# Optimization experiments

Hardware: AMD Instinct MI355X
Metric: run time of the kernel (lower is better)

The kernel has to match this reference:

```python
import jax, jax.numpy as jnp
import numpy as np
from jax import lax

N_WIRES = 4
EPS_BN = 1e-5

def _conv(x, w, b):
    y = lax.conv_general_dilated(x, w, (1, 1), 'SAME',
                                 dimension_numbers=('NCHW', 'OIHW', 'NCHW'))
    return y + b[None, :, None, None]

def _bn2d(x, g, b):
    mu = jnp.mean(x, axis=(0, 2, 3), keepdims=True)
    var = jnp.var(x, axis=(0, 2, 3), keepdims=True)
    return (x - mu) * lax.rsqrt(var + EPS_BN) * g[None, :, None, None] + b[None, :, None, None]

def _maxpool2(x):
    return lax.reduce_window(x, -jnp.inf, lax.max, (1, 1, 2, 2), (1, 1, 2, 2), 'VALID')

def _ry(t):
    c, s = jnp.cos(t / 2), jnp.sin(t / 2)
    return jnp.stack([jnp.stack([c, -s], -1), jnp.stack([s, c], -1)], -2).astype(jnp.complex64)

def _rz(t):
    tc = t.astype(jnp.complex64)
    em, ep = jnp.exp(-0.5j * tc), jnp.exp(0.5j * tc)
    z = jnp.zeros_like(em)
    return jnp.stack([jnpp_stack := jnp.stack([em, z], -1), jnp.stack([z, ep], -1)], -2)

def _rx(t):
    c = jnp.cos(t / 2).astype(jnp.complex64)
    s = (-1j) * jnp.sin(t / 2).astype(jnp.complex64)
    return jnp.stack([jnp.stack([c, s], -1), jnp.stack([s, c], -1)], -2)

def _apply_1q(state, U, q):
    # state: (B,2,2,2,2); U: (2,2) shared or (B,2,2) per-sample
    a = jnp.moveaxis(state, 1 + q, 1)
    if U.ndim == 2:
        a = jnp.einsum('ij,bj...->bi...', U, a)
    else:
        a = jnp.einsum('bij,bj...->bi...', U, a)
    return jnp.moveaxis(a, 1, 1 + q)

def _cnot(state, c, t):
    a = jnp.moveaxis(state, (1 + c, 1 + t), (1, 2))
    a = jnp.stack([a[:, 0], jnp.flip(a[:, 1], axis=1)], axis=1)
    return jnp.moveaxis(a, (1, 2), (1 + c, 1 + t))

def _circuit(scaled, theta, rho):
    # scaled: (B, 4) angles; theta, rho: (4, 3)
    B = scaled.shape[0]
    state = jnp.zeros((B,) + (2,) * N_WIRES, jnp.complex64)
    state = state.at[(slice(None),) + (0,) * N_WIRES].set(1.0 + 0j)
    for i in range(N_WIRES):
        state = _apply_1q(state, _ry(scaled[:, i]), i)
    for i in range(N_WIRES):
        state = _apply_1q(state, _ry(theta[i, 0]), i)
        state = _apply_1q(state, _rz(theta[i, 1]), i)
        state = _apply_1q(state, _rx(theta[i, 2]), i)
    for i in range(N_WIRES - 1):
        state = _cnot(state, i, i + 1)
    for i in range(N_WIRES):
        state = _apply_1q(state, _ry(rho[i, 0]), i)
        state = _apply_1q(state, _rz(rho[i, 1]), i)
        state = _apply_1q(state, _rx(rho[i, 2]), i)
    for i in range(N_WIRES - 1):
        state = _cnot(state, i + 1, i)
    probs = jnp.abs(state) ** 2  # (B,2,2,2,2)
    exps = []
    for i in range(N_WIRES):
        p = jnp.moveaxis(probs, 1 + i, 1)
        exps.append(jnp.sum(p[:, 0], axis=(1, 2, 3)) - jnp.sum(p[:, 1], axis=(1, 2, 3)))
    return jnp.stack(exps, axis=1)  # (B,4)

def setup_inputs() -> dict:
    key = jax.random.key(0)
    ks = jax.random.split(key, 8)
    B = 128
    return {
        'x': jax.random.normal(ks[0], (B, 1, 224, 224), jnp.float32),
        'conv1_w': jax.random.normal(ks[1], (8, 1, 3, 3), jnp.float32) * 0.1,
        'conv1_b': jnp.zeros((8,), jnp.float32),
        'bn1_g': jnp.ones((8,), jnp.float32),
        'bn1_b': jnp.zeros((8,), jnp.float32),
        'conv2_w': jax.random.normal(ks[2], (16, 8, 3, 3), jnp.float32) * 0.1,
        'conv2_b': jnp.zeros((16,), jnp.float32),
        'bn2_g': jnp.ones((16,), jnp.float32),
        'bn2_b': jnp.zeros((16,), jnp.float32),
        'theta': jax.random.normal(ks[3], (4, 3), jnp.float32),
        'rho': jax.random.normal(ks[4], (4, 3), jnp.float32),
        'norm_g': jnp.ones((4,), jnp.float32),
        'norm_b': jnp.zeros((4,), jnp.float32),
    }

def reference(x, conv1_w, conv1_b, bn1_g, bn1_b, conv2_w, conv2_b, bn2_g, bn2_b,
              theta, rho, norm_g, norm_b):
    h = jax.nn.relu(_bn2d(_conv(x, conv1_w, conv1_b), bn1_g, bn1_b))
    h = _maxpool2(h)
    h = jax.nn.relu(_bn2d(_conv(h, conv2_w, conv2_b), bn2_g, bn2_b))
    h = _maxpool2(h)
    feat = jnp.mean(h, axis=(2, 3))          # AdaptiveAvgPool2d((1,1)) + flatten -> (B,16)
    feat = feat[:, :N_WIRES]                  # (B,4)
    scaled = (feat - jnp.mean(feat)) / (jnp.std(feat, ddof=1) + 1e-6) * jnp.pi
    out = _circuit(scaled, theta, rho)        # (B,4) real
    mu = jnp.mean(out, axis=0, keepdims=True)
    var = jnp.var(out, axis=0, keepdims=True)
    return (out - mu) * lax.rsqrt(var + EPS_BN) * norm_g[None, :] + norm_b[None, :]
```

## Files before the change

kernel.cpp:

```cpp
#include <hip/hip_runtime.h>
#include <math.h>

#define H1 224
#define W1 224
#define H2 112
#define W2 112
#define HP 56
#define WP 56

#define NS 32
#define SLOT_STRIDE 64

struct C2 { float re, im; };
__device__ __forceinline__ C2 cmul(C2 a, C2 b) {
    return C2{fmaf(a.re, b.re, -a.im * b.im), fmaf(a.re, b.im, a.im * b.re)};
}
__device__ __forceinline__ C2 cadd(C2 a, C2 b) { return C2{a.re + b.re, a.im + b.im}; }

template <int S>
__device__ __forceinline__ void ap1s(C2* st, C2 u00, C2 u01, C2 u10, C2 u11) {
#pragma unroll
    for (int i = 0; i < 16; i++) {
        if (i & S) continue;
        C2 a0 = st[i], a1 = st[i + S];
        st[i]     = cadd(cmul(u00, a0), cmul(u01, a1));
        st[i + S] = cadd(cmul(u10, a0), cmul(u11, a1));
    }
}
template <int SC, int STT>
__device__ __forceinline__ void cnot_s(C2* st) {
#pragma unroll
    for (int i = 0; i < 16; i++)
        if ((i & SC) && !(i & STT)) { C2 t = st[i]; st[i] = st[i + STT]; st[i + STT] = t; }
}
struct M2 { C2 m[2][2]; };
__device__ __forceinline__ M2 mmul(const M2& A, const M2& B) {
    M2 R;
#pragma unroll
    for (int i = 0; i < 2; i++)
#pragma unroll
        for (int j = 0; j < 2; j++)
            R.m[i][j] = cadd(cmul(A.m[i][0], B.m[0][j]), cmul(A.m[i][1], B.m[1][j]));
    return R;
}
__device__ __forceinline__ M2 combined_u(const float* __restrict__ p) {
    float c0 = cosf(0.5f * p[0]), s0 = sinf(0.5f * p[0]);
    float c1 = cosf(0.5f * p[1]), s1 = sinf(0.5f * p[1]);
    float c2 = cosf(0.5f * p[2]), s2 = sinf(0.5f * p[2]);
    M2 Ry = {{{{c0, 0.f}, {-s0, 0.f}}, {{s0, 0.f}, {c0, 0.f}}}};
    M2 Rz = {{{{c1, -s1}, {0.f, 0.f}}, {{0.f, 0.f}, {c1, s1}}}};
    M2 Rx = {{{{c2, 0.f}, {0.f, -s2}}, {{0.f, -s2}, {c2, 0.f}}}};
    return mmul(Rx, mmul(Rz, Ry));
}

template <int Q>
__device__ __forceinline__ void rows_reduce(float* red, const float* vals, int tid) {
#pragma unroll
    for (int q = 0; q < Q; q++) red[q * 256 + tid] = vals[q];
    __syncthreads();
#pragma unroll
    for (int s = 128; s > 0; s >>= 1) {
        for (int idx = tid; idx < Q * s; idx += 256) {
            int row = idx / s, i = idx - row * s;
            red[row * 256 + i] += red[row * 256 + i + s];
        }
        __syncthreads();
    }
}

__global__ void zero_ws(float* ws, int n) {
    int i = blockIdx.x * blockDim.x + threadIdx.x;
    if (i < n) ws[i] = 0.f;
}

__device__ __forceinline__ float slot_sum(const float* stats, int c) {
    float s = 0.f;
#pragma unroll
    for (int sl = 0; sl < NS; sl++) s += stats[sl * SLOT_STRIDE + c];
    return s;
}

__global__ __launch_bounds__(256, 2) void conv1_pool_stats(
        const float* __restrict__ x, const float* __restrict__ w,
        const float* __restrict__ bias, const float* __restrict__ g1,
        float* __restrict__ stats1p, float* __restrict__ p1ext) {
    __shared__ float red[16 * 256];
    int strip = blockIdx.x;
    int b = blockIdx.y;
    int tid = threadIdx.x;
    int pc = tid & 127;
    int rhalf = tid >> 7;
    int r0 = strip * 16 + rhalf * 8;
    const float* xb = x + (size_t)b * H1 * W1;
    float sums[8], sqs[8], pm[8];
    bool gp[8];
#pragma unroll
    for (int c = 0; c < 8; c++) { sums[c] = 0.f; sqs[c] = 0.f; gp[c] = g1[c] >= 0.f; }
    bool act = pc < W2;
    if (act) {
        bool cl = pc > 0, cr = pc < W2 - 1;
        const float* rp0 = xb + (size_t)r0 * W1 + 2 * pc;
        float al, am0, am1, ar, bl, bm0, bm1, br;
        if (r0 > 0) {
            const float* rp = rp0 - W1;
            float2 m = *(const float2*)rp;
            al = cl ? rp[-1] : 0.f; am0 = m.x; am1 = m.y; ar = cr ? rp[2] : 0.f;
        } else { al = 0.f; am0 = 0.f; am1 = 0.f; ar = 0.f; }
        {
            float2 m = *(const float2*)rp0;
            bl = cl ? rp0[-1] : 0.f; bm0 = m.x; bm1 = m.y; br = cr ? rp0[2] : 0.f;
        }
#pragma unroll
        for (int rr = 0; rr < 8; rr++) {
            float nl = 0.f, nm0 = 0.f, nm1 = 0.f, nr = 0.f;
            int rn = r0 + rr + 1;
            if (rn < H1) {
                const float* rp = rp0 + (size_t)(rr + 1) * W1;
                float2 m = *(const float2*)rp;
                nl = cl ? rp[-1] : 0.f; nm0 = m.x; nm1 = m.y; nr = cr ? rp[2] : 0.f;
            }
            float4 e0 = make_float4(0.f, 0.f, 0.f, 0.f);
            float4 e1 = make_float4(0.f, 0.f, 0.f, 0.f);
#pragma unroll
            for (int c = 0; c < 8; c++) {
                const float* wc = w + c * 9;
                float y0 = bias[c], y1 = bias[c];
                y0 = fmaf(wc[0], al,  y0); y0 = fmaf(wc[1], am0, y0); y0 = fmaf(wc[2], am1, y0);
                y1 = fmaf(wc[0], am0, y1); y1 = fmaf(wc[1], am1, y1); y1 = fmaf(wc[2], ar,  y1);
                y0 = fmaf(wc[3], bl,  y0); y0 = fmaf(wc[4], bm0, y0); y0 = fmaf(wc[5], bm1, y0);
                y1 = fmaf(wc[3], bm0, y1); y1 = fmaf(wc[4], bm1, y1); y1 = fmaf(wc[5], br,  y1);
                y0 = fmaf(wc[6], nl,  y0); y0 = fmaf(wc[7], nm0, y0); y0 = fmaf(wc[8], nm1, y0);
                y1 = fmaf(wc[6], nm0, y1); y1 = fmaf(wc[7], nm1, y1); y1 = fmaf(wc[8], nr,  y1);
                sums[c] += y0 + y1;
                sqs[c] = fmaf(y0, y0, fmaf(y1, y1, sqs[c]));
                float m01 = gp[c] ? fmaxf(y0, y1) : fminf(y0, y1);
                if ((rr & 1) == 0) {
                    pm[c] = m01;
                } else {
                    float e = gp[c] ? fmaxf(pm[c], m01) : fminf(pm[c], m01);
                    if (c == 0) e0.x = e; else if (c == 1) e0.y = e;
                    else if (c == 2) e0.z = e; else if (c == 3) e0.w = e;
                    else if (c == 4) e1.x = e; else if (c == 5) e1.y = e;
                    else if (c == 6) e1.z = e; else e1.w = e;
                }
            }
            if (rr & 1) {
                int pr = (r0 + rr) >> 1;
                float* dst = p1ext + ((((size_t)b * H2 + pr) * W2 + pc) << 3);
                ((float4*)dst)[0] = e0;
                ((float4*)dst)[1] = e1;
            }
            al = bl; am0 = bm0; am1 = bm1; ar = br;
            bl = nl; bm0 = nm0; bm1 = nm1; br = nr;
        }
    }
    float vals[16];
#pragma unroll
    for (int c = 0; c < 8; c++) { vals[c] = sums[c]; vals[8 + c] = sqs[c]; }
    rows_reduce<16>(red, vals, tid);
    if (tid < 16) stats1p[((size_t)(b * 14 + strip) << 4) + tid] = red[tid * 256];
}

__global__ void conv1_stats(const float* __restrict__ x, const float* __restrict__ w,
                            const float* __restrict__ bias, float* __restrict__ stats) {
    __shared__ float red[16 * 256];
    int strip = blockIdx.x;
    int b = blockIdx.y;
    int tid = threadIdx.x;
    const float* xb = x + (size_t)b * H1 * W1;
    float sums[8], sqs[8];
#pragma unroll
    for (int c = 0; c < 8; c++) { sums[c] = 0.f; sqs[c] = 0.f; }
    int col = tid;
    if (col < W1) {
        bool cl = col > 0, cr = col < W1 - 1;
        int row0 = strip * 8;
        float a0, a1, a2, b0, b1, b2, c0, c1, c2;
        {
            int r = row0 - 1;
            if (r >= 0) {
                a0 = cl ? xb[r * W1 + col - 1] : 0.f;
                a1 = xb[r * W1 + col];
                a2 = cr ? xb[r * W1 + col + 1] : 0.f;
            } else { a0 = a1 = a2 = 0.f; }
            r = row0;
            b0 = cl ? xb[r * W1 + col - 1] : 0.f;
            b1 = xb[r * W1 + col];
            b2 = cr ? xb[r * W1 + col + 1] : 0.f;
        }
        for (int rr = 0; rr < 8; rr++) {
            int rn = row0 + rr + 1;
            if (rn < H1) {
                c0 = cl ? xb[rn * W1 + col - 1] : 0.f;
                c1 = xb[rn * W1 + col];
                c2 = cr ? xb[rn * W1 + col + 1] : 0.f;
            } else { c0 = c1 = c2 = 0.f; }
#pragma unroll
            for (int c = 0; c < 8; c++) {
                float acc = bias[c];
                acc = fmaf(w[c * 9 + 0], a0, acc);
                acc = fmaf(w[c * 9 + 1], a1, acc);
                acc = fmaf(w[c * 9 + 2], a2, acc);
                acc = fmaf(w[c * 9 + 3], b0, acc);
                acc = fmaf(w[c * 9 + 4], b1, acc);
                acc = fmaf(w[c * 9 + 5], b2, acc);
                acc = fmaf(w[c * 9 + 6], c0, acc);
                acc = fmaf(w[c * 9 + 7], c1, acc);
                acc = fmaf(w[c * 9 + 8], c2, acc);
                sums[c] += acc;
                sqs[c] = fmaf(acc, acc, sqs[c]);
            }
            a0 = b0; a1 = b1; a2 = b2;
            b0 = c0; b1 = c1; b2 = c2;
        }
    }
    float vals[16];
#pragma unroll
    for (int c = 0; c < 8; c++) { vals[c] = sums[c]; vals[8 + c] = sqs[c]; }
    rows_reduce<16>(red, vals, tid);
    int slot = (b * 28 + strip) & (NS - 1);
    if (tid < 16) atomicAdd(stats + slot * SLOT_STRIDE + tid, red[tid * 256]);
}

template <int PH, int PW>
__device__ __forceinline__ void build_h1_tile(const float* __restrict__ xb,
                                              float (*h1t)[PH][PW],
                                              const float* __restrict__ w1,
                                              const float* __restrict__ b1,
                                              const float* sc1, const float* sh1,
                                              int oy0, int ox0, int tid) {
    for (int i = tid; i < PH * PW; i += 256) {
        int p = i / PW, q = i % PW;
        int hy = oy0 + p, hx = ox0 + q;
        bool ok = (hy >= 0 && hy < H2 && hx >= 0 && hx < W2);
        float xp[5][5];
        if (hy >= 1 && hy <= H2 - 2 && hx >= 1 && hx <= W2 - 2) {
            const float* bp = xb + (2 * hy - 1) * W1 + (2 * hx - 1);
#pragma unroll
            for (int r = 0; r < 5; r++)
#pragma unroll
                for (int c = 0; c < 5; c++) xp[r][c] = bp[r * W1 + c];
        } else if (ok) {
#pragma unroll
            for (int r = 0; r < 5; r++)
#pragma unroll
                for (int c = 0; c < 5; c++) {
                    int gy = 2 * hy - 1 + r, gx = 2 * hx - 1 + c;
                    xp[r][c] = (gy >= 0 && gy < H1 && gx >= 0 && gx < W1) ? xb[gy * W1 + gx] : 0.f;
                }
        }
#pragma unroll
        for (int c = 0; c < 8; c++) {
            float mx = 0.f;
            if (ok) {
                mx = -INFINITY;
#pragma unroll
                for (int dy = 0; dy < 2; dy++)
#pragma unroll
                    for (int dx = 0; dx < 2; dx++) {
                        float acc = b1[c];
#pragma unroll
                        for (int ky = 0; ky < 3; ky++)
#pragma unroll
                            for (int kx = 0; kx < 3; kx++)
                                acc = fmaf(w1[c * 9 + ky * 3 + kx], xp[dy + ky][dx + kx], acc);
                        mx = fmaxf(mx, fmaxf(fmaf(acc, sc1[c], sh1[c]), 0.f));
                    }
            }
            h1t[c][p][q] = mx;
        }
    }
}

__global__ __launch_bounds__(256, 4) void conv2_stats_slim(
        const float* __restrict__ p1ext, const float* __restrict__ g1,
        const float* __restrict__ be1, const float* __restrict__ stats1p, int nblk1,
        const float* __restrict__ w2, const float* __restrict__ b2,
        const float* __restrict__ g2,
        float* __restrict__ stats2p, float* __restrict__ p2ext, float N1) {
    __shared__ __align__(16) float h1t[8][34][34];
    __shared__ float sc1[8], sh1[8];
    int b = blockIdx.z;
    int Y0 = blockIdx.y * 32, X0 = blockIdx.x * 32;
    int ty = threadIdx.y, tx = threadIdx.x;
    int tid = ty * 16 + tx;
    {
        float* scr = (float*)h1t;
        const float4* sp = (const float4*)stats1p;
        int tot4 = nblk1 << 2;
        float4 a0 = make_float4(0.f, 0.f, 0.f, 0.f);
        float4 a1 = a0, a2 = a0, a3 = a0;
        int idx = tid;
        for (; idx + 768 < tot4; idx += 1024) {
            float4 t0 = sp[idx];
            float4 t1 = sp[idx + 256];
            float4 t2 = sp[idx + 512];
            float4 t3 = sp[idx + 768];
            a0.x += t0.x; a0.y += t0.y; a0.z += t0.z; a0.w += t0.w;
            a1.x += t1.x; a1.y += t1.y; a1.z += t1.z; a1.w += t1.w;
            a2.x += t2.x; a2.y += t2.y; a2.z += t2.z; a2.w += t2.w;
            a3.x += t3.x; a3.y += t3.y; a3.z += t3.z; a3.w += t3.w;
        }
        for (; idx < tot4; idx += 256) {
            float4 t = sp[idx];
            a0.x += t.x; a0.y += t.y; a0.z += t.z; a0.w += t.w;
        }
        a0.x += a1.x + a2.x + a3.x;
        a0.y += a1.y + a2.y + a3.y;
        a0.z += a1.z + a2.z + a3.z;
        a0.w += a1.w + a2.w + a3.w;
        ((float4*)scr)[tid] = a0;
        __syncthreads();
        if (tid < 16) {
            int hi = tid >> 2, lo = tid & 3;
            float s = 0.f;
#pragma unroll
            for (int k = 0; k < 64; k++) s += scr[(((hi + (k << 2))) << 2) + lo];
            scr[1024 + tid] = s;
        }
        __syncthreads();
        if (tid < 8) {
            float su = scr[1024 + tid], sq = scr[1024 + 8 + tid];
            float mu = su / N1;
            float var = sq / N1 - mu * mu;
            float sc = g1[tid] * rsqrtf(var + 1e-5f);
            sc1[tid] = sc;
            sh1[tid] = be1[tid] - mu * sc;
        }
        __syncthreads();
    }
    const float* pb = p1ext + (((size_t)b * H2) * W2 << 3);
    for (int i = tid; i < 34 * 34; i += 256) {
        int p = i / 34, q = i % 34;
        int hy = Y0 - 1 + p, hx = X0 - 1 + q;
        if (hy >= 0 && hy < H2 && hx >= 0 && hx < W2) {
            const float* cp = pb + (((size_t)hy * W2 + hx) << 3);
            float4 u = ((const float4*)cp)[0];
            float4 v = ((const float4*)cp)[1];
            h1t[0][p][q] = fmaxf(fmaf(u.x, sc1[0], sh1[0]), 0.f);
            h1t[1][p][q] = fmaxf(fmaf(u.y, sc1[1], sh1[1]), 0.f);
            h1t[2][p][q] = fmaxf(fmaf(u.z, sc1[2], sh1[2]), 0.f);
            h1t[3][p][q] = fmaxf(fmaf(u.w, sc1[3], sh1[3]), 0.f);
            h1t[4][p][q] = fmaxf(fmaf(v.x, sc1[4], sh1[4]), 0.f);
            h1t[5][p][q] = fmaxf(fmaf(v.y, sc1[5], sh1[5]), 0.f);
            h1t[6][p][q] = fmaxf(fmaf(v.z, sc1[6], sh1[6]), 0.f);
            h1t[7][p][q] = fmaxf(fmaf(v.w, sc1[7], sh1[7]), 0.f);
        } else {
#pragma unroll
            for (int c = 0; c < 8; c++) h1t[c][p][q] = 0.f;
        }
    }
    __syncthreads();
    float acc[4][2][2];
#pragma unroll
    for (int co = 0; co < 4; co++)
#pragma unroll
        for (int dy = 0; dy < 2; dy++)
#pragma unroll
            for (int dx = 0; dx < 2; dx++) acc[co][dy][dx] = b2[co];
#pragma unroll
    for (int ci = 0; ci < 8; ci++) {
        float win[4][4];
#pragma unroll
        for (int r = 0; r < 4; r++) {
            const float2* rp = (const float2*)&h1t[ci][2 * ty + r][2 * tx];
            float2 u = rp[0], v = rp[1];
            win[r][0] = u.x; win[r][1] = u.y; win[r][2] = v.x; win[r][3] = v.y;
        }
#pragma unroll
        for (int co = 0; co < 4; co++)
#pragma unroll
            for (int ky = 0; ky < 3; ky++)
#pragma unroll
                for (int kx = 0; kx < 3; kx++) {
                    float wv = w2[co * 72 + ci * 9 + ky * 3 + kx];
#pragma unroll
                    for (int dy = 0; dy < 2; dy++)
#pragma unroll
                        for (int dx = 0; dx < 2; dx++)
                            acc[co][dy][dx] = fmaf(wv, win[dy + ky][dx + kx], acc[co][dy][dx]);
                }
    }
    int cy0 = Y0 + 2 * ty, cx0 = X0 + 2 * tx;
    bool vy0 = cy0 < H2, vy1 = cy0 + 1 < H2, vx0 = cx0 < W2, vx1 = cx0 + 1 < W2;
    float vals[8];
#pragma unroll
    for (int co = 0; co < 4; co++) {
        float s = 0.f, q = 0.f;
        if (vy0 && vx0) { float a = acc[co][0][0]; s += a; q = fmaf(a, a, q); }
        if (vy0 && vx1) { float a = acc[co][0][1]; s += a; q = fmaf(a, a, q); }
        if (vy1 && vx0) { float a = acc[co][1][0]; s += a; q = fmaf(a, a, q); }
        if (vy1 && vx1) { float a = acc[co][1][1]; s += a; q = fmaf(a, a, q); }
        vals[co] = s;
        vals[4 + co] = q;
    }
    {
        int hy = (Y0 >> 1) + ty, hx = (X0 >> 1) + tx;
        if (hy < HP && hx < WP) {
#pragma unroll
            for (int co = 0; co < 4; co++) {
                float mx = fmaxf(fmaxf(acc[co][0][0], acc[co][0][1]),
                                 fmaxf(acc[co][1][0], acc[co][1][1]));
                float mn = fminf(fminf(acc[co][0][0], acc[co][0][1]),
                                 fminf(acc[co][1][0], acc[co][1][1]));
                p2ext[(((size_t)b * 4 + co) * HP + hy) * WP + hx] = (g2[co] >= 0.f) ? mx : mn;
            }
        }
    }
    __syncthreads();
    float* red = (float*)h1t;
    rows_reduce<8>(red, vals, tid);
    int blkid = (blockIdx.z * gridDim.y + blockIdx.y) * gridDim.x + blockIdx.x;
    if (tid < 8) stats2p[((size_t)blkid << 3) + tid] = red[tid * 256];
}

template <bool STORE>
__global__ __launch_bounds__(256, 4) void conv2_stats_fused(
        const float* __restrict__ x, const float* __restrict__ w1,
        const float* __restrict__ b1, const float* __restrict__ g1,
        const float* __restrict__ be1, const float* __restrict__ stats1,
        const float* __restrict__ w2, const float* __restrict__ b2,
        float* __restrict__ stats2,
        float* __restrict__ pmax, float* __restrict__ pmin, float N1) {
    __shared__ __align__(16) float h1t[8][34][34];
    __shared__ float sc1[8], sh1[8];
    int b = blockIdx.z;
    int Y0 = blockIdx.y * 32, X0 = blockIdx.x * 32;
    int ty = threadIdx.y, tx = threadIdx.x;
    int tid = ty * 16 + tx;
    if (tid < 8) {
        float su = slot_sum(stats1, tid), sq = slot_sum(stats1, 8 + tid);
        float mu = su / N1;
        float var = sq / N1 - mu * mu;
        float sc = g1[tid] * rsqrtf(var + 1e-5f);
        sc1[tid] = sc;
        sh1[tid] = be1[tid] - mu * sc;
    }
    __syncthreads();
    const float* xb = x + (size_t)b * H1 * W1;
    build_h1_tile<34, 34>(xb, h1t, w1, b1, sc1, sh1, Y0 - 1, X0 - 1, tid);
    __syncthreads();
    float acc[4][2][2];
#pragma unroll
    for (int co = 0; co < 4; co++)
#pragma unroll
        for (int dy = 0; dy < 2; dy++)
#pragma unroll
            for (int dx = 0; dx < 2; dx++) acc[co][dy][dx] = b2[co];
#pragma unroll
    for (int ci = 0; ci < 8; ci++) {
        float win[4][4];
#pragma unroll
        for (int r = 0; r < 4; r++) {
            const float2* rp = (const float2*)&h1t[ci][2 * ty + r][2 * tx];
            float2 u = rp[0], v = rp[1];
            win[r][0] = u.x; win[r][1] = u.y; win[r][2] = v.x; win[r][3] = v.y;
        }
#pragma unroll
        for (int co = 0; co < 4; co++)
#pragma unroll
            for (int ky = 0; ky < 3; ky++)
#pragma unroll
                for (int kx = 0; kx < 3; kx++) {
                    float wv = w2[co * 72 + ci * 9 + ky * 3 + kx];
#pragma unroll
                    for (int dy = 0; dy < 2; dy++)
#pragma unroll
                        for (int dx = 0; dx < 2; dx++)
                            acc[co][dy][dx] = fmaf(wv, win[dy + ky][dx + kx], acc[co][dy][dx]);
                }
    }
    int cy0 = Y0 + 2 * ty, cx0 = X0 + 2 * tx;
    bool vy0 = cy0 < H2, vy1 = cy0 + 1 < H2, vx0 = cx0 < W2, vx1 = cx0 + 1 < W2;
    float vals[8];
#pragma unroll
    for (int co = 0; co < 4; co++) {
        float s = 0.f, q = 0.f;
        if (vy0 && vx0) { float a = acc[co][0][0]; s += a; q = fmaf(a, a, q); }
        if (vy0 && vx1) { float a = acc[co][0][1]; s += a; q = fmaf(a, a, q); }
        if (vy1 && vx0) { float a = acc[co][1][0]; s += a; q = fmaf(a, a, q); }
        if (vy1 && vx1) { float a = acc[co][1][1]; s += a; q = fmaf(a, a, q); }
        vals[co] = s;
        vals[4 + co] = q;
    }
    if (STORE) {
        int hy = (Y0 >> 1) + ty, hx = (X0 >> 1) + tx;
        if (hy < HP && hx < WP) {
#pragma unroll
            for (int co = 0; co < 4; co++) {
                float mx = fmaxf(fmaxf(acc[co][0][0], acc[co][0][1]),
                                 fmaxf(acc[co][1][0], acc[co][1][1]));
                float mn = fminf(fminf(acc[co][0][0], acc[co][0][1]),
                                 fminf(acc[co][1][0], acc[co][1][1]));
                size_t idx = (((size_t)b * 4 + co) * HP + hy) * WP + hx;
                pmax[idx] = mx;
                pmin[idx] = mn;
            }
        }
    }
    __syncthreads();
    float* red = (float*)h1t;
    rows_reduce<8>(red, vals, tid);
    int slot = ((b * 16) + blockIdx.y * 4 + blockIdx.x) & (NS - 1);
    if (tid < 8) atomicAdd(stats2 + slot * SLOT_STRIDE + tid, red[tid * 256]);
}

__global__ void pool_bn_mean_p(const float* __restrict__ p2ext,
                               const float* __restrict__ g2, const float* __restrict__ be2,
                               const float* __restrict__ stats2p, int nblk2,
                               float* __restrict__ featbuf, float N2) {
    __shared__ float red[1024 + 16];
    int co = blockIdx.x & 3;
    int b = blockIdx.x >> 2;
    int tid = threadIdx.x;
    {
        const float4* sp = (const float4*)stats2p;
        int tot4 = nblk2 << 1;
        float4 a0 = make_float4(0.f, 0.f, 0.f, 0.f);
        float4 a1 = a0;
        int idx = tid;
        for (; idx + 256 < tot4; idx += 512) {
            float4 t0 = sp[idx];
            float4 t1 = sp[idx + 256];
            a0.x += t0.x; a0.y += t0.y; a0.z += t0.z; a0.w += t0.w;
            a1.x += t1.x; a1.y += t1.y; a1.z += t1.z; a1.w += t1.w;
        }
        for (; idx < tot4; idx += 256) {
            float4 t = sp[idx];
            a0.x += t.x; a0.y += t.y; a0.z += t.z; a0.w += t.w;
        }
        a0.x += a1.x; a0.y += a1.y; a0.z += a1.z; a0.w += a1.w;
        ((float4*)red)[tid] = a0;
    }
    __syncthreads();
    if (tid < 8) {
        int hi = tid >> 2, lo = tid & 3;
        float s = 0.f;
#pragma unroll
        for (int k = 0; k < 128; k++) s += red[((hi + (k << 1)) << 2) + lo];
        red[1024 + tid] = s;
    }
    __syncthreads();
    float su = red[1024 + co], sq = red[1024 + 4 + co];
    float mu = su / N2;
    float var = sq / N2 - mu * mu;
    float sc = g2[co] * rsqrtf(var + 1e-5f);
    float sh = be2[co] - mu * sc;
    const float4* P4 = (const float4*)(p2ext + ((size_t)b * 4 + co) * (HP * WP));
    float s = 0.f;
    for (int i = tid; i < (HP * WP) / 4; i += 256) {
        float4 t = P4[i];
        s += fmaxf(fmaf(t.x, sc, sh), 0.f) + fmaxf(fmaf(t.y, sc, sh), 0.f) +
             fmaxf(fmaf(t.z, sc, sh), 0.f) + fmaxf(fmaf(t.w, sc, sh), 0.f);
    }
    __syncthreads();
    red[tid] = s;
    __syncthreads();
    for (int st = 128; st > 0; st >>= 1) {
        if (tid < st) red[tid] += red[tid + st];
        __syncthreads();
    }
    if (tid == 0) featbuf[(size_t)b * 4 + co] = red[0];
}

__global__ void pool_bn_mean(const float* __restrict__ pmax, const float* __restrict__ pmin,
                             const float* __restrict__ g2, const float* __restrict__ be2,
                             const float* __restrict__ stats2,
                             float* __restrict__ featbuf, float N2) {
    __shared__ float red[256];
    int co = blockIdx.x & 3;
    int b = blockIdx.x >> 2;
    int tid = threadIdx.x;
    float su = slot_sum(stats2, co), sq = slot_sum(stats2, 4 + co);
    float mu = su / N2;
    float var = sq / N2 - mu * mu;
    float sc = g2[co] * rsqrtf(var + 1e-5f);
    float sh = be2[co] - mu * sc;
    const float* P = (sc >= 0.f ? pmax : pmin) + ((size_t)b * 4 + co) * (HP * WP);
    float s = 0.f;
    for (int i = tid; i < HP * WP; i += 256) s += fmaxf(fmaf(P[i], sc, sh), 0.f);
    red[tid] = s;
    __syncthreads();
    for (int st = 128; st > 0; st >>= 1) {
        if (tid < st) red[tid] += red[tid + st];
        __syncthreads();
    }
    if (tid == 0) featbuf[(size_t)b * 4 + co] = red[0];
}

__global__ void conv2_final_fused(const float* __restrict__ x, const float* __restrict__ w1,
                                  const float* __restrict__ b1, const float* __restrict__ g1,
                                  const float* __restrict__ be1,
                                  const float* __restrict__ stats1,
                                  const float* __restrict__ w2, const float* __restrict__ b2,
                                  const float* __restrict__ g2, const float* __restrict__ be2,
                                  const float* __restrict__ stats2,
                                  float* __restrict__ featbuf, float N1, float N2) {
    __shared__ __align__(16) float h1t[8][34][34];
    __shared__ float sc1[8], sh1[8];
    __shared__ float sc2[4], sh2[4];
    int b = blockIdx.z;
    int py0 = blockIdx.y * 16, px0 = blockIdx.x * 16;
    int ty = threadIdx.y, tx = threadIdx.x;
    int tid = ty * 16 + tx;
    if (tid < 8) {
        float su = slot_sum(stats1, tid), sq = slot_sum(stats1, 8 + tid);
        float mu = su / N1;
        float var = sq / N1 - mu * mu;
        float sc = g1[tid] * rsqrtf(var + 1e-5f);
        sc1[tid] = sc;
        sh1[tid] = be1[tid] - mu * sc;
    }
    if (tid >= 16 && tid < 20) {
        int j = tid - 16;
        float su = slot_sum(stats2, j), sq = slot_sum(stats2, 4 + j);
        float mu = su / N2;
        float var = sq / N2 - mu * mu;
        float sc = g2[j] * rsqrtf(var + 1e-5f);
        sc2[j] = sc;
        sh2[j] = be2[j] - mu * sc;
    }
    __syncthreads();
    const float* xb = x + (size_t)b * H1 * W1;
    build_h1_tile<34, 34>(xb, h1t, w1, b1, sc1, sh1, 2 * py0 - 1, 2 * px0 - 1, tid);
    __syncthreads();
    bool valid = (py0 + ty < HP) && (px0 + tx < WP);
    float acc[4][2][2];
#pragma unroll
    for (int co = 0; co < 4; co++)
#pragma unroll
        for (int dy = 0; dy < 2; dy++)
#pragma unroll
            for (int dx = 0; dx < 2; dx++) acc[co][dy][dx] = b2[co];
#pragma unroll
    for (int ci = 0; ci < 8; ci++) {
        float win[4][4];
#pragma unroll
        for (int r = 0; r < 4; r++) {
            const float2* rp = (const float2*)&h1t[ci][2 * ty + r][2 * tx];
            float2 u = rp[0], v = rp[1];
            win[r][0] = u.x; win[r][1] = u.y; win[r][2] = v.x; win[r][3] = v.y;
        }
#pragma unroll
        for (int co = 0; co < 4; co++)
#pragma unroll
            for (int ky = 0; ky < 3; ky++)
#pragma unroll
                for (int kx = 0; kx < 3; kx++) {
                    float wv = w2[co * 72 + ci * 9 + ky * 3 + kx];
#pragma unroll
                    for (int dy = 0; dy < 2; dy++)
#pragma unroll
                        for (int dx = 0; dx < 2; dx++)
                            acc[co][dy][dx] = fmaf(wv, win[dy + ky][dx + kx], acc[co][dy][dx]);
                }
    }
    float vals[4];
#pragma unroll
    for (int co = 0; co < 4; co++) {
        float mx = -INFINITY;
#pragma unroll
        for (int dy = 0; dy < 2; dy++)
#pragma unroll
            for (int dx = 0; dx < 2; dx++)
                mx = fmaxf(mx, fmaxf(fmaf(acc[co][dy][dx], sc2[co], sh2[co]), 0.f));
        vals[co] = valid ? mx : 0.f;
    }
    __syncthreads();
    float* red = (float*)h1t;
    rows_reduce<4>(red, vals, tid);
    if (tid < 4) atomicAdd(featbuf + (size_t)b * 4 + tid, red[tid * 256]);
}

__device__ __forceinline__ float bsum(float v, float* lds) {
#pragma unroll
    for (int off = 32; off; off >>= 1) v += __shfl_xor(v, off, 64);
    __syncthreads();
    if ((threadIdx.x & 63) == 0) lds[threadIdx.x >> 6] = v;
    __syncthreads();
    float r = 0.f;
    int nw = (int)(blockDim.x + 63) >> 6;
#pragma clang loop unroll(disable)
    for (int i = 0; i < nw; i++) r += lds[i];
    return r;
}

__global__ void finalize(const float* __restrict__ featbuf, const float* __restrict__ theta,
                         const float* __restrict__ rho, const float* __restrict__ ng,
                         const float* __restrict__ nb, float* __restrict__ out, int B) {
    __shared__ float lds[16];
    int b = threadIdx.x;
    float f[4];
#pragma unroll
    for (int j = 0; j < 4; j++) f[j] = featbuf[b * 4 + j] * (1.f / (HP * WP));
    float n = 4.f * (float)B;
    float mean = bsum(f[0] + f[1] + f[2] + f[3], lds) / n;
    float d2 = 0.f;
#pragma unroll
    for (int j = 0; j < 4; j++) { float d = f[j] - mean; d2 += d * d; }
    float var1 = bsum(d2, lds) / (n - 1.f);
    float stdv = sqrtf(fmaxf(var1, 0.f)) + 1e-6f;
    const float PI = 3.14159265358979323846f;
    float cs[4], sn[4];
#pragma unroll
    for (int j = 0; j < 4; j++) {
        float sc = (f[j] - mean) / stdv * PI;
        cs[j] = cosf(0.5f * sc);
        sn[j] = sinf(0.5f * sc);
    }
    C2 st[16];
    {
        float amp[16];
        amp[1] = sn[3]; amp[0] = cs[3];
#pragma unroll
        for (int k = 0; k < 2; k++) { amp[k + 2] = amp[k] * sn[2]; amp[k] *= cs[2]; }
#pragma unroll
        for (int k = 0; k < 4; k++) { amp[k + 4] = amp[k] * sn[1]; amp[k] *= cs[1]; }
#pragma unroll
        for (int k = 0; k < 8; k++) { amp[k + 8] = amp[k] * sn[0]; amp[k] *= cs[0]; }
#pragma unroll
        for (int i = 0; i < 16; i++) st[i] = C2{amp[i], 0.f};
    }
#pragma clang loop unroll(disable)
    for (int l = 0; l < 2; l++) {
        const float* p = (l == 0) ? theta : rho;
#pragma clang loop unroll(disable)
        for (int i = 0; i < 4; i++) {
            M2 U = combined_u(p + i * 3);
            switch (i) {
            case 0: ap1s<8>(st, U.m[0][0], U.m[0][1], U.m[1][0], U.m[1][1]); break;
            case 1: ap1s<4>(st, U.m[0][0], U.m[0][1], U.m[1][0], U.m[1][1]); break;
            case 2: ap1s<2>(st, U.m[0][0], U.m[0][1], U.m[1][0], U.m[1][1]); break;
            default: ap1s<1>(st, U.m[0][0], U.m[0][1], U.m[1][0], U.m[1][1]); break;
            }
        }
        if (l == 0) { cnot_s<8, 4>(st); cnot_s<4, 2>(st); cnot_s<2, 1>(st); }
        else        { cnot_s<4, 8>(st); cnot_s<2, 4>(st); cnot_s<1, 2>(st); }
    }
    float e[4];
#pragma unroll
    for (int qb = 0; qb < 4; qb++) {
        int m = 8 >> qb;
        float p0 = 0.f, p1 = 0.f;
#pragma unroll
        for (int i = 0; i < 16; i++) {
            float pr = st[i].re * st[i].re + st[i].im * st[i].im;
            if (i & m) p1 += pr; else p0 += pr;
        }
        e[qb] = p0 - p1;
    }
#pragma clang loop unroll(disable)
    for (int j = 0; j < 4; j++) {
        float mu = bsum(e[j], lds) / (float)B;
        float dv = e[j] - mu;
        float v = bsum(dv * dv, lds) / (float)B;
        out[b * 4 + j] = fmaf(dv, rsqrtf(v + 1e-5f) * ng[j], nb[j]);
    }
}

extern "C" void kernel_launch(void* const* d_in, const int* in_sizes, int n_in,
                              void* d_out, int out_size, void* d_ws, size_t ws_size,
                              hipStream_t stream) {
    const float* x     = (const float*)d_in[0];
    const float* w1    = (const float*)d_in[1];
    const float* b1    = (const float*)d_in[2];
    const float* g1    = (const float*)d_in[3];
    const float* be1   = (const float*)d_in[4];
    const float* w2    = (const float*)d_in[5];
    const float* b2    = (const float*)d_in[6];
    const float* g2    = (const float*)d_in[7];
    const float* be2   = (const float*)d_in[8];
    const float* theta = (const float*)d_in[9];
    const float* rho   = (const float*)d_in[10];
    const float* ng    = (const float*)d_in[11];
    const float* nb    = (const float*)d_in[12];
    float* out = (float*)d_out;

    int B = in_sizes[0] / (H1 * W1);

    float N1 = (float)B * H1 * W1;
    float N2 = (float)B * H2 * W2;

    int nblk1 = 14 * B;
    int nblk2 = 16 * B;

    size_t p2n = (size_t)B * 4 * HP * WP;
    size_t p1n = (size_t)B * 8 * H2 * W2;

    size_t offs1p = 0;
    size_t offs2p = offs1p + (size_t)nblk1 * 16;
    size_t offfb  = offs2p + (size_t)nblk2 * 8;
    size_t offp2  = offfb + (size_t)B * 4;
    size_t offp1  = offp2 + p2n;
    size_t needA  = (offp1 + p1n) * sizeof(float);

    size_t common = (size_t)(2 * NS * SLOT_STRIDE) + (size_t)B * 4;
    size_t needB = (common + 2 * p2n) * sizeof(float);

    bool tierA = ws_size >= needA;
    bool tierB = !tierA && ws_size >= needB;

    float* ws = (float*)d_ws;

    if (tierA) {
        float* stats1p = ws + offs1p;
        float* stats2p = ws + offs2p;
        float* featbuf = ws + offfb;
        float* p2ext   = ws + offp2;
        float* p1ext   = ws + offp1;
        conv1_pool_stats<<<dim3(14, B), 256, 0, stream>>>(x, w1, b1, g1, stats1p, p1ext);
        conv2_stats_slim<<<dim3(4, 4, B), dim3(16, 16), 0, stream>>>(
            p1ext, g1, be1, stats1p, nblk1, w2, b2, g2, stats2p, p2ext, N1);
        pool_bn_mean_p<<<B * 4, 256, 0, stream>>>(p2ext, g2, be2, stats2p, nblk2, featbuf, N2);
        finalize<<<1, B, 0, stream>>>(featbuf, theta, rho, ng, nb, out, B);
    } else if (tierB) {
        float* stats1 = ws;
        float* stats2 = ws + NS * SLOT_STRIDE;
        float* featbuf = ws + 2 * NS * SLOT_STRIDE;
        float* bufs = featbuf + (size_t)B * 4;
        float* pmax = bufs;
        float* pmin = bufs + p2n;
        int nz = (int)common;
        zero_ws<<<(nz + 255) / 256, 256, 0, stream>>>(ws, nz);
        conv1_stats<<<dim3(28, B), 256, 0, stream>>>(x, w1, b1, stats1);
        conv2_stats_fused<true><<<dim3(4, 4, B), dim3(16, 16), 0, stream>>>(
            x, w1, b1, g1, be1, stats1, w2, b2, stats2, pmax, pmin, N1);
        pool_bn_mean<<<B * 4, 256, 0, stream>>>(pmax, pmin, g2, be2, stats2, featbuf, N2);
        finalize<<<1, B, 0, stream>>>(featbuf, theta, rho, ng, nb, out, B);
    } else {
        float* stats1 = ws;
        float* stats2 = ws + NS * SLOT_STRIDE;
        float* featbuf = ws + 2 * NS * SLOT_STRIDE;
        int nz = (int)common;
        zero_ws<<<(nz + 255) / 256, 256, 0, stream>>>(ws, nz);
        conv1_stats<<<dim3(28, B), 256, 0, stream>>>(x, w1, b1, stats1);
        conv2_stats_fused<false><<<dim3(4, 4, B), dim3(16, 16), 0, stream>>>(
            x, w1, b1, g1, be1, stats1, w2, b2, stats2, nullptr, nullptr, N1);
        conv2_final_fused<<<dim3(4, 4, B), dim3(16, 16), 0, stream>>>(
            x, w1, b1, g1, be1, stats1, w2, b2, g2, be2, stats2, featbuf, N1, N2);
        finalize<<<1, B, 0, stream>>>(featbuf, theta, rho, ng, nb, out, B);
    }
}
```

Before: 173.0 us.

## Fuse pipeline into single cooperative persistent kernel with grid syncs

Replaces the four-kernel tier-A pipeline (conv1+pool+stats, conv2+stats, pool/BN mean, finalize) with one cooperative kernel. It loops over work items per phase and separates phases with grid.sync, so per-launch overhead and inter-kernel gaps go away. BN1 affine terms are computed once by block 0 and broadcast through workspace instead of being recomputed in every conv2 block. The costs are grid-sync latency, idle blocks during the serial phases, and lower occupancy from the larger shared-memory footprint. Fallback launches of finalize now use 256 threads.

```diff
diff --git a/kernel.cpp b/kernel.cpp
--- a/kernel.cpp
+++ b/kernel.cpp
@@ -1,5 +1,8 @@
 #include <hip/hip_runtime.h>
+#include <hip/hip_cooperative_groups.h>
 #include <math.h>
+
+namespace cg = cooperative_groups;
 
 #define H1 224
 #define W1 224
@@ -80,22 +83,19 @@
     return s;
 }
 
-__global__ __launch_bounds__(256, 2) void conv1_pool_stats(
-        const float* __restrict__ x, const float* __restrict__ w,
-        const float* __restrict__ bias, const float* __restrict__ g1,
-        float* __restrict__ stats1p, float* __restrict__ p1ext) {
-    __shared__ float red[16 * 256];
-    int strip = blockIdx.x;
-    int b = blockIdx.y;
-    int tid = threadIdx.x;
+
+__device__ __forceinline__ void conv1_item_body(
+        int b, int strip, const float* __restrict__ x, const float* __restrict__ w,
+        const float* __restrict__ bias, const bool* gp,
+        float* __restrict__ stats1p, float* __restrict__ p1ext,
+        float* red, int tid, int witem) {
     int pc = tid & 127;
     int rhalf = tid >> 7;
     int r0 = strip * 16 + rhalf * 8;
     const float* xb = x + (size_t)b * H1 * W1;
     float sums[8], sqs[8], pm[8];
-    bool gp[8];
-#pragma unroll
-    for (int c = 0; c < 8; c++) { sums[c] = 0.f; sqs[c] = 0.f; gp[c] = g1[c] >= 0.f; }
+#pragma unroll
+    for (int c = 0; c < 8; c++) { sums[c] = 0.f; sqs[c] = 0.f; }
     bool act = pc < W2;
     if (act) {
         bool cl = pc > 0, cr = pc < W2 - 1;
@@ -158,8 +158,449 @@
 #pragma unroll
     for (int c = 0; c < 8; c++) { vals[c] = sums[c]; vals[8 + c] = sqs[c]; }
     rows_reduce<16>(red, vals, tid);
-    if (tid < 16) stats1p[((size_t)(b * 14 + strip) << 4) + tid] = red[tid * 256];
-}
+    if (tid < 16) stats1p[((size_t)witem << 4) + tid] = red[tid * 256];
+}
+
+__device__ __forceinline__ void conv2_item_body(
+        int b, int Y0, int X0, const float* __restrict__ p1ext,
+        const float* sc1, const float* sh1,
+        const float* __restrict__ w2, const float* __restrict__ b2,
+        const float* __restrict__ g2,
+        float* __restrict__ stats2p, float* __restrict__ p2ext,
+        float* smem, int tid, int witem) {
+    float (*h1t)[34][34] = (float(*)[34][34])smem;
+    int ty = tid >> 4, tx = tid & 15;
+    const float* pb = p1ext + (((size_t)b * H2) * W2 << 3);
+    for (int i = tid; i < 34 * 34; i += 256) {
+        int p = i / 34, q = i % 34;
+        int hy = Y0 - 1 + p, hx = X0 - 1 + q;
+        if (hy >= 0 && hy < H2 && hx >= 0 && hx < W2) {
+            const float* cp = pb + (((size_t)hy * W2 + hx) << 3);
+            float4 u = ((const float4*)cp)[0];
+            float4 v = ((const float4*)cp)[1];
+            h1t[0][p][q] = fmaxf(fmaf(u.x, sc1[0], sh1[0]), 0.f);
+            h1t[1][p][q] = fmaxf(fmaf(u.y, sc1[1], sh1[1]), 0.f);
+            h1t[2][p][q] = fmaxf(fmaf(u.z, sc1[2], sh1[2]), 0.f);
+            h1t[3][p][q] = fmaxf(fmaf(u.w, sc1[3], sh1[3]), 0.f);
+            h1t[4][p][q] = fmaxf(fmaf(v.x, sc1[4], sh1[4]), 0.f);
+            h1t[5][p][q] = fmaxf(fmaf(v.y, sc1[5], sh1[5]), 0.f);
+            h1t[6][p][q] = fmaxf(fmaf(v.z, sc1[6], sh1[6]), 0.f);
+            h1t[7][p][q] = fmaxf(fmaf(v.w, sc1[7], sh1[7]), 0.f);
+        } else {
+#pragma unroll
+            for (int c = 0; c < 8; c++) h1t[c][p][q] = 0.f;
+        }
+    }
+    __syncthreads();
+    float acc[4][2][2];
+#pragma unroll
+    for (int co = 0; co < 4; co++)
+#pragma unroll
+        for (int dy = 0; dy < 2; dy++)
+#pragma unroll
+            for (int dx = 0; dx < 2; dx++) acc[co][dy][dx] = b2[co];
+#pragma unroll
+    for (int ci = 0; ci < 8; ci++) {
+        float win[4][4];
+#pragma unroll
+        for (int r = 0; r < 4; r++) {
+            const float2* rp = (const float2*)&h1t[ci][2 * ty + r][2 * tx];
+            float2 u = rp[0], v = rp[1];
+            win[r][0] = u.x; win[r][1] = u.y; win[r][2] = v.x; win[r][3] = v.y;
+        }
+#pragma unroll
+        for (int co = 0; co < 4; co++)
+#pragma unroll
+            for (int ky = 0; ky < 3; ky++)
+#pragma unroll
+                for (int kx = 0; kx < 3; kx++) {
+                    float wv = w2[co * 72 + ci * 9 + ky * 3 + kx];
+#pragma unroll
+                    for (int dy = 0; dy < 2; dy++)
+#pragma unroll
+                        for (int dx = 0; dx < 2; dx++)
+                            acc[co][dy][dx] = fmaf(wv, win[dy + ky][dx + kx], acc[co][dy][dx]);
+                }
+    }
+    int cy0 = Y0 + 2 * ty, cx0 = X0 + 2 * tx;
+    bool vy0 = cy0 < H2, vy1 = cy0 + 1 < H2, vx0 = cx0 < W2, vx1 = cx0 + 1 < W2;
+    float vals[8];
+#pragma unroll
+    for (int co = 0; co < 4; co++) {
+        float s = 0.f, q = 0.f;
+        if (vy0 && vx0) { float a = acc[co][0][0]; s += a; q = fmaf(a, a, q); }
+        if (vy0 && vx1) { float a = acc[co][0][1]; s += a; q = fmaf(a, a, q); }
+        if (vy1 && vx0) { float a = acc[co][1][0]; s += a; q = fmaf(a, a, q); }
+        if (vy1 && vx1) { float a = acc[co][1][1]; s += a; q = fmaf(a, a, q); }
+        vals[co] = s;
+        vals[4 + co] = q;
+    }
+    {
+        int hy = (Y0 >> 1) + ty, hx = (X0 >> 1) + tx;
+        if (hy < HP && hx < WP) {
+#pragma unroll
+            for (int co = 0; co < 4; co++) {
+                float mx = fmaxf(fmaxf(acc[co][0][0], acc[co][0][1]),
+                                 fmaxf(acc[co][1][0], acc[co][1][1]));
+                float mn = fminf(fminf(acc[co][0][0], acc[co][0][1]),
+                                 fminf(acc[co][1][0], acc[co][1][1]));
+                p2ext[(((size_t)b * 4 + co) * HP + hy) * WP + hx] = (g2[co] >= 0.f) ? mx : mn;
+            }
+        }
+    }
+    __syncthreads();
+    rows_reduce<8>(smem, vals, tid);
+    if (tid < 8) stats2p[((size_t)witem << 3) + tid] = smem[tid * 256];
+}
+
+__device__ __forceinline__ void pool_item_body(
+        int b, int co, const float* __restrict__ p2ext,
+        const float* __restrict__ g2, const float* __restrict__ be2,
+        const float* __restrict__ stats2p, int nblk2,
+        float* __restrict__ featbuf, float N2, float* red, int tid) {
+    {
+        const float4* sp = (const float4*)stats2p;
+        int tot4 = nblk2 << 1;
+        float4 a0 = make_float4(0.f, 0.f, 0.f, 0.f);
+        float4 a1 = a0;
+        int idx = tid;
+        for (; idx + 256 < tot4; idx += 512) {
+            float4 t0 = sp[idx];
+            float4 t1 = sp[idx + 256];
+            a0.x += t0.x; a0.y += t0.y; a0.z += t0.z; a0.w += t0.w;
+            a1.x += t1.x; a1.y += t1.y; a1.z += t1.z; a1.w += t1.w;
+        }
+        for (; idx < tot4; idx += 256) {
+            float4 t = sp[idx];
+            a0.x += t.x; a0.y += t.y; a0.z += t.z; a0.w += t.w;
+        }
+        a0.x += a1.x; a0.y += a1.y; a0.z += a1.z; a0.w += a1.w;
+        ((float4*)red)[tid] = a0;
+    }
+    __syncthreads();
+    if (tid < 8) {
+        int hi = tid >> 2, lo = tid & 3;
+        float s = 0.f;
+#pragma unroll
+        for (int k = 0; k < 128; k++) s += red[((hi + (k << 1)) << 2) + lo];
+        red[1024 + tid] = s;
+    }
+    __syncthreads();
+    float su = red[1024 + co], sq = red[1024 + 4 + co];
+    float mu = su / N2;
+    float var = sq / N2 - mu * mu;
+    float sc = g2[co] * rsqrtf(var + 1e-5f);
+    float sh = be2[co] - mu * sc;
+    const float4* P4 = (const float4*)(p2ext + ((size_t)b * 4 + co) * (HP * WP));
+    float s = 0.f;
+    for (int i = tid; i < (HP * WP) / 4; i += 256) {
+        float4 t = P4[i];
+        s += fmaxf(fmaf(t.x, sc, sh), 0.f) + fmaxf(fmaf(t.y, sc, sh), 0.f) +
+             fmaxf(fmaf(t.z, sc, sh), 0.f) + fmaxf(fmaf(t.w, sc, sh), 0.f);
+    }
+    __syncthreads();
+    red[tid] = s;
+    __syncthreads();
+    for (int st = 128; st > 0; st >>= 1) {
+        if (tid < st) red[tid] += red[tid + st];
+        __syncthreads();
+    }
+    if (tid == 0) featbuf[(size_t)b * 4 + co] = red[0];
+}
+
+__device__ __forceinline__ float bsum(float v, float* lds) {
+#pragma unroll
+    for (int off = 32; off; off >>= 1) v += __shfl_xor(v, off, 64);
+    __syncthreads();
+    if ((threadIdx.x & 63) == 0) lds[threadIdx.x >> 6] = v;
+    __syncthreads();
+    float r = 0.f;
+    int nw = (int)(blockDim.x + 63) >> 6;
+#pragma clang loop unroll(disable)
+    for (int i = 0; i < nw; i++) r += lds[i];
+    return r;
+}
+
+__device__ __forceinline__ void finalize_body(
+        const float* __restrict__ featbuf, const float* __restrict__ theta,
+        const float* __restrict__ rho, const float* __restrict__ ng,
+        const float* __restrict__ nb, float* __restrict__ out, int B, float* lds) {
+    int b = threadIdx.x;
+    bool act = b < B;
+    float f[4];
+#pragma unroll
+    for (int j = 0; j < 4; j++) f[j] = act ? featbuf[b * 4 + j] * (1.f / (HP * WP)) : 0.f;
+    float n = 4.f * (float)B;
+    float mean = bsum(f[0] + f[1] + f[2] + f[3], lds) / n;
+    float d2 = 0.f;
+    if (act) {
+#pragma unroll
+        for (int j = 0; j < 4; j++) { float d = f[j] - mean; d2 += d * d; }
+    }
+    float var1 = bsum(d2, lds) / (n - 1.f);
+    float stdv = sqrtf(fmaxf(var1, 0.f)) + 1e-6f;
+    const float PI = 3.14159265358979323846f;
+    float cs[4], sn[4];
+#pragma unroll
+    for (int j = 0; j < 4; j++) {
+        float sc = (f[j] - mean) / stdv * PI;
+        cs[j] = cosf(0.5f * sc);
+        sn[j] = sinf(0.5f * sc);
+    }
+    C2 st[16];
+    {
+        float amp[16];
+        amp[1] = sn[3]; amp[0] = cs[3];
+#pragma unroll
+        for (int k = 0; k < 2; k++) { amp[k + 2] = amp[k] * sn[2]; amp[k] *= cs[2]; }
+#pragma unroll
+        for (int k = 0; k < 4; k++) { amp[k + 4] = amp[k] * sn[1]; amp[k] *= cs[1]; }
+#pragma unroll
+        for (int k = 0; k < 8; k++) { amp[k + 8] = amp[k] * sn[0]; amp[k] *= cs[0]; }
+#pragma unroll
+        for (int i = 0; i < 16; i++) st[i] = C2{amp[i], 0.f};
+    }
+#pragma clang loop unroll(disable)
+    for (int l = 0; l < 2; l++) {
+        const float* p = (l == 0) ? theta : rho;
+#pragma clang loop unroll(disable)
+        for (int i = 0; i < 4; i++) {
+            M2 U = combined_u(p + i * 3);
+            switch (i) {
+            case 0: ap1s<8>(st, U.m[0][0], U.m[0][1], U.m[1][0], U.m[1][1]); break;
+            case 1: ap1s<4>(st, U.m[0][0], U.m[0][1], U.m[1][0], U.m[1][1]); break;
+            case 2: ap1s<2>(st, U.m[0][0], U.m[0][1], U.m[1][0], U.m[1][1]); break;
+            default: ap1s<1>(st, U.m[0][0], U.m[0][1], U.m[1][0], U.m[1][1]); break;
+            }
+        }
+        if (l == 0) { cnot_s<8, 4>(st); cnot_s<4, 2>(st); cnot_s<2, 1>(st); }
+        else        { cnot_s<4, 8>(st); cnot_s<2, 4>(st); cnot_s<1, 2>(st); }
+    }
+    float e[4];
+#pragma unroll
+    for (int qb = 0; qb < 4; qb++) {
+        int m = 8 >> qb;
+        float p0 = 0.f, p1 = 0.f;
+#pragma unroll
+        for (int i = 0; i < 16; i++) {
+            float pr = st[i].re * st[i].re + st[i].im * st[i].im;
+            if (i & m) p1 += pr; else p0 += pr;
+        }
+        e[qb] = p0 - p1;
+    }
+#pragma clang loop unroll(disable)
+    for (int j = 0; j < 4; j++) {
+        float mu = bsum(act ? e[j] : 0.f, lds) / (float)B;
+        float dv = e[j] - mu;
+        float v = bsum(act ? dv * dv : 0.f, lds) / (float)B;
+        if (act) out[b * 4 + j] = fmaf(dv, rsqrtf(v + 1e-5f) * ng[j], nb[j]);
+    }
+}
+
+__global__ __launch_bounds__(256, 4) void mega_all(
+        const float* __restrict__ x, const float* __restrict__ w1,
+        const float* __restrict__ b1, const float* __restrict__ g1,
+        const float* __restrict__ be1,
+        const float* __restrict__ w2, const float* __restrict__ b2,
+        const float* __restrict__ g2, const float* __restrict__ be2,
+        const float* __restrict__ theta, const float* __restrict__ rho,
+        const float* __restrict__ ng, const float* __restrict__ nb,
+        float* __restrict__ stats1p, float* __restrict__ stats2p,
+        float* __restrict__ aff1, float* __restrict__ featbuf,
+        float* __restrict__ p2ext, float* __restrict__ p1ext,
+        float* __restrict__ out, int B) {
+    cg::grid_group grid = cg::this_grid();
+    __shared__ __align__(16) float smem[8 * 34 * 34];
+    __shared__ float sc1s[8], sh1s[8];
+    int tid = threadIdx.x;
+    int bid = blockIdx.x;
+    int gsz = gridDim.x;
+    float N1 = (float)B * H1 * W1;
+    float N2 = (float)B * H2 * W2;
+
+    {
+        bool gp[8];
+#pragma unroll
+        for (int c = 0; c < 8; c++) gp[c] = g1[c] >= 0.f;
+        int n1 = 14 * B;
+        for (int w = bid; w < n1; w += gsz) {
+            __syncthreads();
+            int b = w / 14, strip = w - b * 14;
+            conv1_item_body(b, strip, x, w1, b1, gp, stats1p, p1ext, smem, tid, w);
+        }
+    }
+    __threadfence();
+    grid.sync();
+
+    if (bid == 0) {
+        float* scr = smem;
+        const float4* sp = (const float4*)stats1p;
+        int tot4 = (14 * B) << 2;
+        float4 a0 = make_float4(0.f, 0.f, 0.f, 0.f);
+        float4 a1 = a0, a2 = a0, a3 = a0;
+        int idx = tid;
+        for (; idx + 768 < tot4; idx += 1024) {
+            float4 t0 = sp[idx];
+            float4 t1 = sp[idx + 256];
+            float4 t2 = sp[idx + 512];
+            float4 t3 = sp[idx + 768];
+            a0.x += t0.x; a0.y += t0.y; a0.z += t0.z; a0.w += t0.w;
+            a1.x += t1.x; a1.y += t1.y; a1.z += t1.z; a1.w += t1.w;
+            a2.x += t2.x; a2.y += t2.y; a2.z += t2.z; a2.w += t2.w;
+            a3.x += t3.x; a3.y += t3.y; a3.z += t3.z; a3.w += t3.w;
+        }
+        for (; idx < tot4; idx += 256) {
+            float4 t = sp[idx];
+            a0.x += t.x; a0.y += t.y; a0.z += t.z; a0.w += t.w;
+        }
+        a0.x += a1.x + a2.x + a3.x;
+        a0.y += a1.y + a2.y + a3.y;
+        a0.z += a1.z + a2.z + a3.z;
+        a0.w += a1.w + a2.w + a3.w;
+        ((float4*)scr)[tid] = a0;
+        __syncthreads();
+        if (tid < 16) {
+            int hi = tid >> 2, lo = tid & 3;
+            float s = 0.f;
+#pragma unroll
+            for (int k = 0; k < 64; k++) s += scr[((hi + (k << 2)) << 2) + lo];
+            scr[1024 + tid] = s;
+        }
+        __syncthreads();
+        if (tid < 8) {
+            float su = scr[1024 + tid], sq = scr[1024 + 8 + tid];
+            float mu = su / N1;
+            float var = sq / N1 - mu * mu;
+            float sc = g1[tid] * rsqrtf(var + 1e-5f);
+            aff1[tid] = sc;
+            aff1[8 + tid] = be1[tid] - mu * sc;
+        }
+    }
+    __threadfence();
+    grid.sync();
+
+    {
+        if (tid < 8) { sc1s[tid] = aff1[tid]; sh1s[tid] = aff1[8 + tid]; }
+        __syncthreads();
+        int n2 = 16 * B;
+        for (int w = bid; w < n2; w += gsz) {
+            __syncthreads();
+            int b = w >> 4, t = w & 15;
+            conv2_item_body(b, (t >> 2) * 32, (t & 3) * 32, p1ext, sc1s, sh1s,
+                            w2, b2, g2, stats2p, p2ext, smem, tid, w);
+        }
+    }
+    __threadfence();
+    grid.sync();
+
+    {
+        int n3 = 4 * B;
+        for (int w = bid; w < n3; w += gsz) {
+            __syncthreads();
+            pool_item_body(w >> 2, w & 3, p2ext, g2, be2, stats2p, 16 * B,
+                           featbuf, N2, smem, tid);
+        }
+    }
+    __threadfence();
+    grid.sync();
+
+    if (bid == 0) {
+        __syncthreads();
+        finalize_body(featbuf, theta, rho, ng, nb, out, B, smem);
+    }
+}
+
+
+__global__ __launch_bounds__(256, 2) void conv1_pool_stats(
+        const float* __restrict__ x, const float* __restrict__ w,
+        const float* __restrict__ bias, const float* __restrict__ g1,
+        float* __restrict__ stats1p, float* __restrict__ p1ext) {
+    __shared__ float red[16 * 256];
+    int strip = blockIdx.x;
+    int b = blockIdx.y;
+    int tid = threadIdx.x;
+    bool gp[8];
+#pragma unroll
+    for (int c = 0; c < 8; c++) gp[c] = g1[c] >= 0.f;
+    conv1_item_body(b, strip, x, w, bias, gp, stats1p, p1ext, red, tid, b * 14 + strip);
+}
+
+__global__ __launch_bounds__(256, 4) void conv2_stats_slim(
+        const float* __restrict__ p1ext, const float* __restrict__ g1,
+        const float* __restrict__ be1, const float* __restrict__ stats1p, int nblk1,
+        const float* __restrict__ w2, const float* __restrict__ b2,
+        const float* __restrict__ g2,
+        float* __restrict__ stats2p, float* __restrict__ p2ext, float N1) {
+    __shared__ __align__(16) float smem[8 * 34 * 34];
+    __shared__ float sc1[8], sh1[8];
+    int b = blockIdx.z;
+    int tid = threadIdx.y * 16 + threadIdx.x;
+    {
+        float* scr = smem;
+        const float4* sp = (const float4*)stats1p;
+        int tot4 = nblk1 << 2;
+        float4 a0 = make_float4(0.f, 0.f, 0.f, 0.f);
+        float4 a1 = a0, a2 = a0, a3 = a0;
+        int idx = tid;
+        for (; idx + 768 < tot4; idx += 1024) {
+            float4 t0 = sp[idx];
+            float4 t1 = sp[idx + 256];
+            float4 t2 = sp[idx + 512];
+            float4 t3 = sp[idx + 768];
+            a0.x += t0.x; a0.y += t0.y; a0.z += t0.z; a0.w += t0.w;
+            a1.x += t1.x; a1.y += t1.y; a1.z += t1.z; a1.w += t1.w;
+            a2.x += t2.x; a2.y += t2.y; a2.z += t2.z; a2.w += t2.w;
+            a3.x += t3.x; a3.y += t3.y; a3.z += t3.z; a3.w += t3.w;
+        }
+        for (; idx < tot4; idx += 256) {
+            float4 t = sp[idx];
+            a0.x += t.x; a0.y += t.y; a0.z += t.z; a0.w += t.w;
+        }
+        a0.x += a1.x + a2.x + a3.x;
+        a0.y += a1.y + a2.y + a3.y;
+        a0.z += a1.z + a2.z + a3.z;
+        a0.w += a1.w + a2.w + a3.w;
+        ((float4*)scr)[tid] = a0;
+        __syncthreads();
+        if (tid < 16) {
+            int hi = tid >> 2, lo = tid & 3;
+            float s = 0.f;
+#pragma unroll
+            for (int k = 0; k < 64; k++) s += scr[((hi + (k << 2)) << 2) + lo];
+            scr[1024 + tid] = s;
+        }
+        __syncthreads();
+        if (tid < 8) {
+            float su = scr[1024 + tid], sq = scr[1024 + 8 + tid];
+            float mu = su / N1;
+            float var = sq / N1 - mu * mu;
+            float sc = g1[tid] * rsqrtf(var + 1e-5f);
+            sc1[tid] = sc;
+            sh1[tid] = be1[tid] - mu * sc;
+        }
+        __syncthreads();
+    }
+    int blkid = (blockIdx.z * gridDim.y + blockIdx.y) * gridDim.x + blockIdx.x;
+    conv2_item_body(b, blockIdx.y * 32, blockIdx.x * 32, p1ext, sc1, sh1,
+                    w2, b2, g2, stats2p, p2ext, smem, tid, blkid);
+}
+
+__global__ void pool_bn_mean_p(const float* __restrict__ p2ext,
+                               const float* __restrict__ g2, const float* __restrict__ be2,
+                               const float* __restrict__ stats2p, int nblk2,
+                               float* __restrict__ featbuf, float N2) {
+    __shared__ float red[1024 + 16];
+    pool_item_body(blockIdx.x >> 2, blockIdx.x & 3, p2ext, g2, be2, stats2p, nblk2,
+                   featbuf, N2, red, threadIdx.x);
+}
+
+__global__ void finalize(const float* __restrict__ featbuf, const float* __restrict__ theta,
+                         const float* __restrict__ rho, const float* __restrict__ ng,
+                         const float* __restrict__ nb, float* __restrict__ out, int B) {
+    __shared__ float lds[16];
+    finalize_body(featbuf, theta, rho, ng, nb, out, B, lds);
+}
+
 
 __global__ void conv1_stats(const float* __restrict__ x, const float* __restrict__ w,
                             const float* __restrict__ bias, float* __restrict__ stats) {
@@ -270,148 +711,6 @@
             h1t[c][p][q] = mx;
         }
     }
-}
-
-__global__ __launch_bounds__(256, 4) void conv2_stats_slim(
-        const float* __restrict__ p1ext, const float* __restrict__ g1,
-        const float* __restrict__ be1, const float* __restrict__ stats1p, int nblk1,
-        const float* __restrict__ w2, const float* __restrict__ b2,
-        const float* __restrict__ g2,
-        float* __restrict__ stats2p, float* __restrict__ p2ext, float N1) {
-    __shared__ __align__(16) float h1t[8][34][34];
-    __shared__ float sc1[8], sh1[8];
-    int b = blockIdx.z;
-    int Y0 = blockIdx.y * 32, X0 = blockIdx.x * 32;
-    int ty = threadIdx.y, tx = threadIdx.x;
-    int tid = ty * 16 + tx;
-    {
-        float* scr = (float*)h1t;
-        const float4* sp = (const float4*)stats1p;
-        int tot4 = nblk1 << 2;
-        float4 a0 = make_float4(0.f, 0.f, 0.f, 0.f);
-        float4 a1 = a0, a2 = a0, a3 = a0;
-        int idx = tid;
-        for (; idx + 768 < tot4; idx += 1024) {
-            float4 t0 = sp[idx];
-            float4 t1 = sp[idx + 256];
-            float4 t2 = sp[idx + 512];
-            float4 t3 = sp[idx + 768];
-            a0.x += t0.x; a0.y += t0.y; a0.z += t0.z; a0.w += t0.w;
-            a1.x += t1.x; a1.y += t1.y; a1.z += t1.z; a1.w += t1.w;
-            a2.x += t2.x; a2.y += t2.y; a2.z += t2.z; a2.w += t2.w;
-            a3.x += t3.x; a3.y += t3.y; a3.z += t3.z; a3.w += t3.w;
-        }
-        for (; idx < tot4; idx += 256) {
-            float4 t = sp[idx];
-            a0.x += t.x; a0.y += t.y; a0.z += t.z; a0.w += t.w;
-        }
-        a0.x += a1.x + a2.x + a3.x;
-        a0.y += a1.y + a2.y + a3.y;
-        a0.z += a1.z + a2.z + a3.z;
-        a0.w += a1.w + a2.w + a3.w;
-        ((float4*)scr)[tid] = a0;
-        __syncthreads();
-        if (tid < 16) {
-            int hi = tid >> 2, lo = tid & 3;
-            float s = 0.f;
-#pragma unroll
-            for (int k = 0; k < 64; k++) s += scr[(((hi + (k << 2))) << 2) + lo];
-            scr[1024 + tid] = s;
-        }
-        __syncthreads();
-        if (tid < 8) {
-            float su = scr[1024 + tid], sq = scr[1024 + 8 + tid];
-            float mu = su / N1;
-            float var = sq / N1 - mu * mu;
-            float sc = g1[tid] * rsqrtf(var + 1e-5f);
-            sc1[tid] = sc;
-            sh1[tid] = be1[tid] - mu * sc;
-        }
-        __syncthreads();
-    }
-    const float* pb = p1ext + (((size_t)b * H2) * W2 << 3);
-    for (int i = tid; i < 34 * 34; i += 256) {
-        int p = i / 34, q = i % 34;
-        int hy = Y0 - 1 + p, hx = X0 - 1 + q;
-        if (hy >= 0 && hy < H2 && hx >= 0 && hx < W2) {
-            const float* cp = pb + (((size_t)hy * W2 + hx) << 3);
-            float4 u = ((const float4*)cp)[0];
-            float4 v = ((const float4*)cp)[1];
-            h1t[0][p][q] = fmaxf(fmaf(u.x, sc1[0], sh1[0]), 0.f);
-            h1t[1][p][q] = fmaxf(fmaf(u.y, sc1[1], sh1[1]), 0.f);
-            h1t[2][p][q] = fmaxf(fmaf(u.z, sc1[2], sh1[2]), 0.f);
-            h1t[3][p][q] = fmaxf(fmaf(u.w, sc1[3], sh1[3]), 0.f);
-            h1t[4][p][q] = fmaxf(fmaf(v.x, sc1[4], sh1[4]), 0.f);
-            h1t[5][p][q] = fmaxf(fmaf(v.y, sc1[5], sh1[5]), 0.f);
-            h1t[6][p][q] = fmaxf(fmaf(v.z, sc1[6], sh1[6]), 0.f);
-            h1t[7][p][q] = fmaxf(fmaf(v.w, sc1[7], sh1[7]), 0.f);
-        } else {
-#pragma unroll
-            for (int c = 0; c < 8; c++) h1t[c][p][q] = 0.f;
-        }
-    }
-    __syncthreads();
-    float acc[4][2][2];
-#pragma unroll
-    for (int co = 0; co < 4; co++)
-#pragma unroll
-        for (int dy = 0; dy < 2; dy++)
-#pragma unroll
-            for (int dx = 0; dx < 2; dx++) acc[co][dy][dx] = b2[co];
-#pragma unroll
-    for (int ci = 0; ci < 8; ci++) {
-        float win[4][4];
-#pragma unroll
-        for (int r = 0; r < 4; r++) {
-            const float2* rp = (const float2*)&h1t[ci][2 * ty + r][2 * tx];
-            float2 u = rp[0], v = rp[1];
-            win[r][0] = u.x; win[r][1] = u.y; win[r][2] = v.x; win[r][3] = v.y;
-        }
-#pragma unroll
-        for (int co = 0; co < 4; co++)
-#pragma unroll
-            for (int ky = 0; ky < 3; ky++)
-#pragma unroll
-                for (int kx = 0; kx < 3; kx++) {
-                    float wv = w2[co * 72 + ci * 9 + ky * 3 + kx];
-#pragma unroll
-                    for (int dy = 0; dy < 2; dy++)
-#pragma unroll
-                        for (int dx = 0; dx < 2; dx++)
-                            acc[co][dy][dx] = fmaf(wv, win[dy + ky][dx + kx], acc[co][dy][dx]);
-                }
-    }
-    int cy0 = Y0 + 2 * ty, cx0 = X0 + 2 * tx;
-    bool vy0 = cy0 < H2, vy1 = cy0 + 1 < H2, vx0 = cx0 < W2, vx1 = cx0 + 1 < W2;
-    float vals[8];
-#pragma unroll
-    for (int co = 0; co < 4; co++) {
-        float s = 0.f, q = 0.f;
-        if (vy0 && vx0) { float a = acc[co][0][0]; s += a; q = fmaf(a, a, q); }
-        if (vy0 && vx1) { float a = acc[co][0][1]; s += a; q = fmaf(a, a, q); }
-        if (vy1 && vx0) { float a = acc[co][1][0]; s += a; q = fmaf(a, a, q); }
-        if (vy1 && vx1) { float a = acc[co][1][1]; s += a; q = fmaf(a, a, q); }
-        vals[co] = s;
-        vals[4 + co] = q;
-    }
-    {
-        int hy = (Y0 >> 1) + ty, hx = (X0 >> 1) + tx;
-        if (hy < HP && hx < WP) {
-#pragma unroll
-            for (int co = 0; co < 4; co++) {
-                float mx = fmaxf(fmaxf(acc[co][0][0], acc[co][0][1]),
-                                 fmaxf(acc[co][1][0], acc[co][1][1]));
-                float mn = fminf(fminf(acc[co][0][0], acc[co][0][1]),
-                                 fminf(acc[co][1][0], acc[co][1][1]));
-                p2ext[(((size_t)b * 4 + co) * HP + hy) * WP + hx] = (g2[co] >= 0.f) ? mx : mn;
-            }
-        }
-    }
-    __syncthreads();
-    float* red = (float*)h1t;
-    rows_reduce<8>(red, vals, tid);
-    int blkid = (blockIdx.z * gridDim.y + blockIdx.y) * gridDim.x + blockIdx.x;
-    if (tid < 8) stats2p[((size_t)blkid << 3) + tid] = red[tid * 256];
 }
 
 template <bool STORE>
@@ -503,64 +802,6 @@
     rows_reduce<8>(red, vals, tid);
     int slot = ((b * 16) + blockIdx.y * 4 + blockIdx.x) & (NS - 1);
     if (tid < 8) atomicAdd(stats2 + slot * SLOT_STRIDE + tid, red[tid * 256]);
-}
-
-__global__ void pool_bn_mean_p(const float* __restrict__ p2ext,
-                               const float* __restrict__ g2, const float* __restrict__ be2,
-                               const float* __restrict__ stats2p, int nblk2,
-                               float* __restrict__ featbuf, float N2) {
-    __shared__ float red[1024 + 16];
-    int co = blockIdx.x & 3;
-    int b = blockIdx.x >> 2;
-    int tid = threadIdx.x;
-    {
-        const float4* sp = (const float4*)stats2p;
-        int tot4 = nblk2 << 1;
-        float4 a0 = make_float4(0.f, 0.f, 0.f, 0.f);
-        float4 a1 = a0;
-        int idx = tid;
-        for (; idx + 256 < tot4; idx += 512) {
-            float4 t0 = sp[idx];
-            float4 t1 = sp[idx + 256];
-            a0.x += t0.x; a0.y += t0.y; a0.z += t0.z; a0.w += t0.w;
-            a1.x += t1.x; a1.y += t1.y; a1.z += t1.z; a1.w += t1.w;
-        }
-        for (; idx < tot4; idx += 256) {
-            float4 t = sp[idx];
-            a0.x += t.x; a0.y += t.y; a0.z += t.z; a0.w += t.w;
-        }
-        a0.x += a1.x; a0.y += a1.y; a0.z += a1.z; a0.w += a1.w;
-        ((float4*)red)[tid] = a0;
-    }
-    __syncthreads();
-    if (tid < 8) {
-        int hi = tid >> 2, lo = tid & 3;
-        float s = 0.f;
-#pragma unroll
-        for (int k = 0; k < 128; k++) s += red[((hi + (k << 1)) << 2) + lo];
-        red[1024 + tid] = s;
-    }
-    __syncthreads();
-    float su = red[1024 + co], sq = red[1024 + 4 + co];
-    float mu = su / N2;
-    float var = sq / N2 - mu * mu;
-    float sc = g2[co] * rsqrtf(var + 1e-5f);
-    float sh = be2[co] - mu * sc;
-    const float4* P4 = (const float4*)(p2ext + ((size_t)b * 4 + co) * (HP * WP));
-    float s = 0.f;
-    for (int i = tid; i < (HP * WP) / 4; i += 256) {
-        float4 t = P4[i];
-        s += fmaxf(fmaf(t.x, sc, sh), 0.f) + fmaxf(fmaf(t.y, sc, sh), 0.f) +
-             fmaxf(fmaf(t.z, sc, sh), 0.f) + fmaxf(fmaf(t.w, sc, sh), 0.f);
-    }
-    __syncthreads();
-    red[tid] = s;
-    __syncthreads();
-    for (int st = 128; st > 0; st >>= 1) {
-        if (tid < st) red[tid] += red[tid + st];
-        __syncthreads();
-    }
-    if (tid == 0) featbuf[(size_t)b * 4 + co] = red[0];
 }
 
 __global__ void pool_bn_mean(const float* __restrict__ pmax, const float* __restrict__ pmin,
@@ -672,92 +913,6 @@
     if (tid < 4) atomicAdd(featbuf + (size_t)b * 4 + tid, red[tid * 256]);
 }
 
-__device__ __forceinline__ float bsum(float v, float* lds) {
-#pragma unroll
-    for (int off = 32; off; off >>= 1) v += __shfl_xor(v, off, 64);
-    __syncthreads();
-    if ((threadIdx.x & 63) == 0) lds[threadIdx.x >> 6] = v;
-    __syncthreads();
-    float r = 0.f;
-    int nw = (int)(blockDim.x + 63) >> 6;
-#pragma clang loop unroll(disable)
-    for (int i = 0; i < nw; i++) r += lds[i];
-    return r;
-}
-
-__global__ void finalize(const float* __restrict__ featbuf, const float* __restrict__ theta,
-                         const float* __restrict__ rho, const float* __restrict__ ng,
-                         const float* __restrict__ nb, float* __restrict__ out, int B) {
-    __shared__ float lds[16];
-    int b = threadIdx.x;
-    float f[4];
-#pragma unroll
-    for (int j = 0; j < 4; j++) f[j] = featbuf[b * 4 + j] * (1.f / (HP * WP));
-    float n = 4.f * (float)B;
-    float mean = bsum(f[0] + f[1] + f[2] + f[3], lds) / n;
-    float d2 = 0.f;
-#pragma unroll
-    for (int j = 0; j < 4; j++) { float d = f[j] - mean; d2 += d * d; }
-    float var1 = bsum(d2, lds) / (n - 1.f);
-    float stdv = sqrtf(fmaxf(var1, 0.f)) + 1e-6f;
-    const float PI = 3.14159265358979323846f;
-    float cs[4], sn[4];
-#pragma unroll
-    for (int j = 0; j < 4; j++) {
-        float sc = (f[j] - mean) / stdv * PI;
-        cs[j] = cosf(0.5f * sc);
-        sn[j] = sinf(0.5f * sc);
-    }
-    C2 st[16];
-    {
-        float amp[16];
-        amp[1] = sn[3]; amp[0] = cs[3];
-#pragma unroll
-        for (int k = 0; k < 2; k++) { amp[k + 2] = amp[k] * sn[2]; amp[k] *= cs[2]; }
-#pragma unroll
-        for (int k = 0; k < 4; k++) { amp[k + 4] = amp[k] * sn[1]; amp[k] *= cs[1]; }
-#pragma unroll
-        for (int k = 0; k < 8; k++) { amp[k + 8] = amp[k] * sn[0]; amp[k] *= cs[0]; }
-#pragma unroll
-        for (int i = 0; i < 16; i++) st[i] = C2{amp[i], 0.f};
-    }
-#pragma clang loop unroll(disable)
-    for (int l = 0; l < 2; l++) {
-        const float* p = (l == 0) ? theta : rho;
-#pragma clang loop unroll(disable)
-        for (int i = 0; i < 4; i++) {
-            M2 U = combined_u(p + i * 3);
-            switch (i) {
-            case 0: ap1s<8>(st, U.m[0][0], U.m[0][1], U.m[1][0], U.m[1][1]); break;
-            case 1: ap1s<4>(st, U.m[0][0], U.m[0][1], U.m[1][0], U.m[1][1]); break;
-            case 2: ap1s<2>(st, U.m[0][0], U.m[0][1], U.m[1][0], U.m[1][1]); break;
-            default: ap1s<1>(st, U.m[0][0], U.m[0][1], U.m[1][0], U.m[1][1]); break;
-            }
-        }
-        if (l == 0) { cnot_s<8, 4>(st); cnot_s<4, 2>(st); cnot_s<2, 1>(st); }
-        else        { cnot_s<4, 8>(st); cnot_s<2, 4>(st); cnot_s<1, 2>(st); }
-    }
-    float e[4];
-#pragma unroll
-    for (int qb = 0; qb < 4; qb++) {
-        int m = 8 >> qb;
-        float p0 = 0.f, p1 = 0.f;
-#pragma unroll
-        for (int i = 0; i < 16; i++) {
-            float pr = st[i].re * st[i].re + st[i].im * st[i].im;
-            if (i & m) p1 += pr; else p0 += pr;
-        }
-        e[qb] = p0 - p1;
-    }
-#pragma clang loop unroll(disable)
-    for (int j = 0; j < 4; j++) {
-        float mu = bsum(e[j], lds) / (float)B;
-        float dv = e[j] - mu;
-        float v = bsum(dv * dv, lds) / (float)B;
-        out[b * 4 + j] = fmaf(dv, rsqrtf(v + 1e-5f) * ng[j], nb[j]);
-    }
-}
-
 extern "C" void kernel_launch(void* const* d_in, const int* in_sizes, int n_in,
                               void* d_out, int out_size, void* d_ws, size_t ws_size,
                               hipStream_t stream) {
@@ -789,7 +944,8 @@
 
     size_t offs1p = 0;
     size_t offs2p = offs1p + (size_t)nblk1 * 16;
-    size_t offfb  = offs2p + (size_t)nblk2 * 8;
+    size_t offaff = offs2p + (size_t)nblk2 * 8;
+    size_t offfb  = offaff + 16;
     size_t offp2  = offfb + (size_t)B * 4;
     size_t offp1  = offp2 + p2n;
     size_t needA  = (offp1 + p1n) * sizeof(float);
@@ -800,9 +956,40 @@
     bool tierA = ws_size >= needA;
     bool tierB = !tierA && ws_size >= needB;
 
+    static int coopGrid = -2;
+    if (coopGrid == -2) {
+        int dev = 0;
+        (void)hipGetDevice(&dev);
+        int coop = 0;
+        (void)hipDeviceGetAttribute(&coop, hipDeviceAttributeCooperativeLaunch, dev);
+        int mb = 0, cus = 0;
+        if (coop) {
+            (void)hipOccupancyMaxActiveBlocksPerMultiprocessor(&mb, mega_all, 256, 0);
+            (void)hipDeviceGetAttribute(&cus, hipDeviceAttributeMultiprocessorCount, dev);
+        }
+        coopGrid = (coop && mb > 0 && cus > 0) ? mb * cus : 0;
+    }
+
     float* ws = (float*)d_ws;
 
-    if (tierA) {
+    if (tierA && coopGrid > 0) {
+        float* stats1p = ws + offs1p;
+        float* stats2p = ws + offs2p;
+        float* aff1    = ws + offaff;
+        float* featbuf = ws + offfb;
+        float* p2ext   = ws + offp2;
+        float* p1ext   = ws + offp1;
+        int g = coopGrid;
+        if (g > nblk2) g = nblk2;
+        void* args[] = {
+            (void*)&x, (void*)&w1, (void*)&b1, (void*)&g1, (void*)&be1,
+            (void*)&w2, (void*)&b2, (void*)&g2, (void*)&be2,
+            (void*)&theta, (void*)&rho, (void*)&ng, (void*)&nb,
+            (void*)&stats1p, (void*)&stats2p, (void*)&aff1, (void*)&featbuf,
+            (void*)&p2ext, (void*)&p1ext, (void*)&out, (void*)&B
+        };
+        (void)hipLaunchCooperativeKernel(mega_all, dim3(g), dim3(256), args, 0, stream);
+    } else if (tierA) {
         float* stats1p = ws + offs1p;
         float* stats2p = ws + offs2p;
         float* featbuf = ws + offfb;
@@ -812,7 +999,7 @@
         conv2_stats_slim<<<dim3(4, 4, B), dim3(16, 16), 0, stream>>>(
             p1ext, g1, be1, stats1p, nblk1, w2, b2, g2, stats2p, p2ext, N1);
         pool_bn_mean_p<<<B * 4, 256, 0, stream>>>(p2ext, g2, be2, stats2p, nblk2, featbuf, N2);
-        finalize<<<1, B, 0, stream>>>(featbuf, theta, rho, ng, nb, out, B);
+        finalize<<<1, 256, 0, stream>>>(featbuf, theta, rho, ng, nb, out, B);
     } else if (tierB) {
         float* stats1 = ws;
         float* stats2 = ws + NS * SLOT_STRIDE;
@@ -826,7 +1013,7 @@
         conv2_stats_fused<true><<<dim3(4, 4, B), dim3(16, 16), 0, stream>>>(
             x, w1, b1, g1, be1, stats1, w2, b2, stats2, pmax, pmin, N1);
         pool_bn_mean<<<B * 4, 256, 0, stream>>>(pmax, pmin, g2, be2, stats2, featbuf, N2);
-        finalize<<<1, B, 0, stream>>>(featbuf, theta, rho, ng, nb, out, B);
+        finalize<<<1, 256, 0, stream>>>(featbuf, theta, rho, ng, nb, out, B);
     } else {
         float* stats1 = ws;
         float* stats2 = ws + NS * SLOT_STRIDE;
@@ -838,6 +1025,6 @@
             x, w1, b1, g1, be1, stats1, w2, b2, stats2, nullptr, nullptr, N1);
         conv2_final_fused<<<dim3(4, 4, B), dim3(16, 16), 0, stream>>>(
             x, w1, b1, g1, be1, stats1, w2, b2, g2, be2, stats2, featbuf, N1, N2);
-        finalize<<<1, B, 0, stream>>>(featbuf, theta, rho, ng, nb, out, B);
-    }
-}
+        finalize<<<1, 256, 0, stream>>>(featbuf, theta, rho, ng, nb, out, B);
+    }
+}
```

After: 642.7 us. +271.5%, slower.
